# Kernel tuning notes

Measured on AMD Instinct MI355X. Metric: run time of the kernel, lower is better.

## Reference

```python
import jax, jax.numpy as jnp
import numpy as np

B, S, H = 512, 100, 768
LAMB = 0.8

def setup_inputs() -> dict:
    key = jax.random.key(0)
    k1, k2, k3, k4 = jax.random.split(key, 4)
    scale = 1.0 / np.sqrt(H)
    return {
        "sent_vec": jax.random.normal(k1, (B, S, H), dtype=jnp.float32),
        "mask_cls": jnp.ones((B, S), dtype=jnp.int32),
        "W_cont": jax.random.normal(k2, (1, H), dtype=jnp.float32) * scale,
        "W_sim": jax.random.normal(k3, (H, H), dtype=jnp.float32) * scale,
        "W_rel": jax.random.normal(k4, (H, H), dtype=jnp.float32) * scale,
        "b_matrix": jnp.zeros((1, 1), dtype=jnp.float32),
    }

def reference(sent_vec, mask_cls, W_cont, W_sim, W_rel, b_matrix):
    # sent_vec: [B,S,H], mask_cls: [B,S] (all ones -> true_dim == S)
    m = mask_cls.astype(sent_vec.dtype)                       # [B,S]
    mask2 = m[:, :, None] * m[:, None, :]                     # mask_my_own [B,S,S]

    # Score_Cont[b,i,j] = W_cont . sent_vec[b,i]
    cont = jnp.einsum('h,bih->bi', W_cont[0], sent_vec)       # [B,S]
    # Score_Sim[b,i,j] = sent_i W_sim sent_j^T, masked
    sim = jnp.einsum('bih,hk,bjk->bij', sent_vec, W_sim, sent_vec) * mask2
    # Score_rel[b,i,j] = sent_i W_rel d_rep, masked
    d_rep = sent_vec.mean(axis=1)                             # [B,H]
    rel = jnp.einsum('bih,hk,bk->bi', sent_vec, W_rel, d_rep) # [B,S]

    q = jax.nn.sigmoid(rel[:, :, None] * mask2 + cont[:, :, None] + sim + b_matrix[0, 0])
    q = q * mask2                                             # [B,S,S]

    # D = diag(column sums of q); q @ D^{-1} divides columns by sum_vec
    sum_vec = q.sum(axis=1)                                   # [B,S]
    qD = q / sum_vec[:, None, :]                              # [B,S,S]

    I = jnp.eye(S, dtype=q.dtype)
    M = I[None, :, :] - LAMB * qD                             # [B,S,S]
    y = jnp.full((B, S, 1), 1.0 / S, dtype=q.dtype)
    # Final_score = (1-lamb) * inv(I - lamb q D^-1) @ y  (solve == inverse@mm)
    score = (1.0 - LAMB) * jnp.linalg.solve(M, y)[:, :, 0]    # [B,S]
    return score
```

## Files before the change

kernel.cpp:

```cpp
#include <hip/hip_runtime.h>
#include <math.h>

#define BB 512
#define SS 100
#define HH 768

typedef __bf16 bf16x8 __attribute__((ext_vector_type(8)));
typedef __bf16 bf16x4 __attribute__((ext_vector_type(4)));
typedef float f32x4 __attribute__((ext_vector_type(4)));
typedef float f32x16 __attribute__((ext_vector_type(16)));

__device__ __forceinline__ void gld16(const void* g, void* l) {
    __builtin_amdgcn_global_load_lds((const __attribute__((address_space(1))) char*)g,
                                     (__attribute__((address_space(3))) char*)l, 16, 0, 0);
}

__global__ __launch_bounds__(256) void k_drep(const float* __restrict__ X,
                                              float* __restrict__ drep) {
    int b = blockIdx.x, g = blockIdx.y;
    int lane = threadIdx.x & 63, w = threadIdx.x >> 6;
    const float4* xb = (const float4*)(X + (size_t)b * SS * HH);
    int c4 = g * 64 + lane;
    float4 s = {0.f, 0.f, 0.f, 0.f};
    for (int r = w; r < SS; r += 4) {
        float4 v = xb[r * 192 + c4];
        s.x += v.x; s.y += v.y; s.z += v.z; s.w += v.w;
    }
    __shared__ float4 red[4][64];
    red[w][lane] = s;
    __syncthreads();
    if (w == 0) {
        float4 a0 = red[0][lane], a1 = red[1][lane], a2 = red[2][lane], a3 = red[3][lane];
        float4 o;
        o.x = (a0.x + a1.x + a2.x + a3.x) * (1.0f / SS);
        o.y = (a0.y + a1.y + a2.y + a3.y) * (1.0f / SS);
        o.z = (a0.z + a1.z + a2.z + a3.z) * (1.0f / SS);
        o.w = (a0.w + a1.w + a2.w + a3.w) * (1.0f / SS);
        ((float4*)(drep + (size_t)b * HH))[c4] = o;
    }
}

__global__ __launch_bounds__(256) void k_gemm_nt(const float* __restrict__ A,
                                                 const float* __restrict__ Bm,
                                                 float* __restrict__ C,
                                                 int N, int K) {
    __shared__ float As[64 * 20];
    __shared__ float Bs[64 * 20];
    int tid = threadIdx.x;
    int ty = tid >> 4, tx = tid & 15;
    int m0 = blockIdx.y * 64, n0 = blockIdx.x * 64;
    int lr = tid >> 2, lc = (tid & 3) * 4;
    float acc[4][4] = {};
    for (int kt = 0; kt < K; kt += 16) {
        *(float4*)(As + lr * 20 + lc) = *(const float4*)(A + (size_t)(m0 + lr) * K + kt + lc);
        *(float4*)(Bs + lr * 20 + lc) = *(const float4*)(Bm + (size_t)(n0 + lr) * K + kt + lc);
        __syncthreads();
        #pragma unroll
        for (int k = 0; k < 16; k += 2) {
            float2 ar[4], br[4];
            #pragma unroll
            for (int ii = 0; ii < 4; ++ii) ar[ii] = *(const float2*)(As + (ty + 16 * ii) * 20 + k);
            #pragma unroll
            for (int jj = 0; jj < 4; ++jj) br[jj] = *(const float2*)(Bs + (tx + 16 * jj) * 20 + k);
            #pragma unroll
            for (int ii = 0; ii < 4; ++ii)
                #pragma unroll
                for (int jj = 0; jj < 4; ++jj)
                    acc[ii][jj] = fmaf(ar[ii].y, br[jj].y, fmaf(ar[ii].x, br[jj].x, acc[ii][jj]));
        }
        __syncthreads();
    }
    #pragma unroll
    for (int ii = 0; ii < 4; ++ii)
        #pragma unroll
        for (int jj = 0; jj < 4; ++jj)
            C[(size_t)(m0 + ty + 16 * ii) * N + n0 + tx + 16 * jj] = acc[ii][jj];
}

__global__ __launch_bounds__(256) void k_splitw(const float* __restrict__ W,
                                                __bf16* __restrict__ th,
                                                __bf16* __restrict__ tl) {
    __shared__ float tile[32][33];
    int bn = blockIdx.x * 32, bk = blockIdx.y * 32;
    int tx = threadIdx.x & 31, ty = threadIdx.x >> 5;
    for (int r = ty; r < 32; r += 8)
        tile[r][tx] = W[(size_t)(bk + r) * HH + bn + tx];
    __syncthreads();
    for (int r = ty; r < 32; r += 8) {
        float v = tile[tx][r];
        __bf16 hv = (__bf16)v;
        size_t idx = (size_t)(bn + r) * HH + bk + tx;
        th[idx] = hv;
        tl[idx] = (__bf16)(v - (float)hv);
    }
}

__global__ __launch_bounds__(512) void k_split_contrel(const float* __restrict__ X,
                                                       const float* __restrict__ Wc,
                                                       const float* __restrict__ tmat,
                                                       const float* __restrict__ bmat,
                                                       __bf16* __restrict__ Xh,
                                                       __bf16* __restrict__ Xl,
                                                       float* __restrict__ avec,
                                                       int b_off) {
    __shared__ float4 u4[192];
    int lb = blockIdx.x, half = blockIdx.y;
    int b = b_off + lb;
    int tid = threadIdx.x, lane = tid & 63, w = tid >> 6;
    for (int c = tid; c < 192; c += 512) {
        float4 wc = ((const float4*)Wc)[c];
        float4 tm = ((const float4*)(tmat + (size_t)b * HH))[c];
        float4 o = {wc.x + tm.x, wc.y + tm.y, wc.z + tm.z, wc.w + tm.w};
        u4[c] = o;
    }
    __syncthreads();
    float b00 = bmat[0];
    const float4* xb = (const float4*)(X + (size_t)b * SS * HH);
    bf16x4* xh4 = (bf16x4*)(Xh + (size_t)lb * SS * HH);
    bf16x4* xl4 = (bf16x4*)(Xl + (size_t)lb * SS * HH);
    int rend = half * 50 + 50;
    for (int r = half * 50 + w; r < rend; r += 8) {
        float s = 0.f;
        #pragma unroll
        for (int cc = 0; cc < 3; ++cc) {
            int c = cc * 64 + lane;
            float4 v = xb[r * 192 + c];
            float4 uu = u4[c];
            s = fmaf(v.x, uu.x, fmaf(v.y, uu.y, fmaf(v.z, uu.z, fmaf(v.w, uu.w, s))));
            bf16x4 hv, lv;
            hv[0] = (__bf16)v.x; lv[0] = (__bf16)(v.x - (float)hv[0]);
            hv[1] = (__bf16)v.y; lv[1] = (__bf16)(v.y - (float)hv[1]);
            hv[2] = (__bf16)v.z; lv[2] = (__bf16)(v.z - (float)hv[2]);
            hv[3] = (__bf16)v.w; lv[3] = (__bf16)(v.w - (float)hv[3]);
            xh4[r * 192 + c] = hv;
            xl4[r * 192 + c] = lv;
        }
        #pragma unroll
        for (int off = 32; off > 0; off >>= 1) s += __shfl_down(s, off);
        if (lane == 0) avec[(size_t)b * SS + r] = s + b00;
    }
}

__global__ __launch_bounds__(256) void k_gemm1_mfma(const __bf16* __restrict__ Ah_g,
                                                    const __bf16* __restrict__ Al_g,
                                                    const __bf16* __restrict__ Bh_g,
                                                    const __bf16* __restrict__ Bl_g,
                                                    __bf16* __restrict__ Yh,
                                                    __bf16* __restrict__ Yl) {
    __shared__ __align__(16) __bf16 lds[4 * 4096];
    __bf16* As_h = lds;
    __bf16* As_l = lds + 4096;
    __bf16* Bs_h = lds + 8192;
    __bf16* Bs_l = lds + 12288;
    const int tid = threadIdx.x;
    const int wave = tid >> 6, lane = tid & 63;
    const int wy = wave >> 1, wx = wave & 1;
    const size_t m0 = (size_t)blockIdx.y * 128;
    const int n0 = blockIdx.x * 128;

    const int srow = wave * 32 + (lane >> 2);
    const int scol = ((lane & 3) ^ ((lane >> 3) & 3)) * 8;
    const int lds_base = wave * 1024;

    const int arow = wy * 64 + (lane & 31);
    const int brow = wx * 64 + (lane & 31);
    const int sw = (lane >> 1) & 3;

    f32x16 acc[2][2] = {};
    for (int kt = 0; kt < HH; kt += 32) {
        const size_t ga0 = (m0 + srow) * HH + kt + scol;
        const size_t ga1 = ga0 + (size_t)16 * HH;
        const size_t gb0 = (size_t)(n0 + srow) * HH + kt + scol;
        const size_t gb1 = gb0 + (size_t)16 * HH;
        gld16(Ah_g + ga0, As_h + lds_base);
        gld16(Ah_g + ga1, As_h + lds_base + 512);
        gld16(Al_g + ga0, As_l + lds_base);
        gld16(Al_g + ga1, As_l + lds_base + 512);
        gld16(Bh_g + gb0, Bs_h + lds_base);
        gld16(Bh_g + gb1, Bs_h + lds_base + 512);
        gld16(Bl_g + gb0, Bs_l + lds_base);
        gld16(Bl_g + gb1, Bs_l + lds_base + 512);
        __syncthreads();
        #pragma unroll
        for (int kh = 0; kh < 2; ++kh) {
            const int ko = (((kh << 1) + (lane >> 5)) ^ sw) << 3;
            bf16x8 fah[2], fal[2], fbh[2], fbl[2];
            #pragma unroll
            for (int t = 0; t < 2; ++t) {
                fah[t] = *(const bf16x8*)(As_h + (arow + t * 32) * 32 + ko);
                fal[t] = *(const bf16x8*)(As_l + (arow + t * 32) * 32 + ko);
                fbh[t] = *(const bf16x8*)(Bs_h + (brow + t * 32) * 32 + ko);
                fbl[t] = *(const bf16x8*)(Bs_l + (brow + t * 32) * 32 + ko);
            }
            #pragma unroll
            for (int ti = 0; ti < 2; ++ti)
                #pragma unroll
                for (int tj = 0; tj < 2; ++tj) {
                    acc[ti][tj] = __builtin_amdgcn_mfma_f32_32x32x16_bf16(fal[ti], fbh[tj], acc[ti][tj], 0, 0, 0);
                    acc[ti][tj] = __builtin_amdgcn_mfma_f32_32x32x16_bf16(fah[ti], fbl[tj], acc[ti][tj], 0, 0, 0);
                    acc[ti][tj] = __builtin_amdgcn_mfma_f32_32x32x16_bf16(fah[ti], fbh[tj], acc[ti][tj], 0, 0, 0);
                }
        }
        __syncthreads();
    }
    const int rbase = 4 * (lane >> 5);
    const int colb = lane & 31;
    #pragma unroll
    for (int ti = 0; ti < 2; ++ti) {
        #pragma unroll
        for (int tj = 0; tj < 2; ++tj) {
            int col = n0 + wx * 64 + tj * 32 + colb;
            #pragma unroll
            for (int r = 0; r < 16; ++r) {
                int row = wy * 64 + ti * 32 + (r & 3) + 8 * (r >> 2) + rbase;
                float v = acc[ti][tj][r];
                __bf16 hv = (__bf16)v;
                size_t idx = (m0 + row) * HH + col;
                Yh[idx] = hv;
                Yl[idx] = (__bf16)(v - (float)hv);
            }
        }
    }
}

__global__ __launch_bounds__(256) void k_gemm2_mfma(const __bf16* __restrict__ Yh,
                                                    const __bf16* __restrict__ Yl,
                                                    const __bf16* __restrict__ Xh,
                                                    const __bf16* __restrict__ Xl,
                                                    const float* __restrict__ avec,
                                                    float* __restrict__ q, int b_off) {
    __shared__ __align__(16) __bf16 lds[4 * 4096];
    __shared__ float av_s[SS];
    __bf16* As_h = lds;
    __bf16* As_l = lds + 4096;
    __bf16* Bs_h = lds + 8192;
    __bf16* Bs_l = lds + 12288;
    const int bl = blockIdx.x;
    const int b = b_off + bl;
    const __bf16* Ah_g = Yh + (size_t)bl * SS * HH;
    const __bf16* Al_g = Yl + (size_t)bl * SS * HH;
    const __bf16* Bh_g = Xh + (size_t)bl * SS * HH;
    const __bf16* Bl_g = Xl + (size_t)bl * SS * HH;
    const int tid = threadIdx.x;
    const int wave = tid >> 6, lane = tid & 63;
    const int wy = wave >> 1, wx = wave & 1;
    if (tid < SS) av_s[tid] = avec[(size_t)b * SS + tid];

    const int srow_raw = wave * 32 + (lane >> 2);
    const int scol = ((lane & 3) ^ ((lane >> 3) & 3)) * 8;
    const int lds_base = wave * 1024;
    const int r0 = srow_raw < SS ? srow_raw : SS - 1;
    const int r1 = (srow_raw + 16) < SS ? (srow_raw + 16) : SS - 1;

    const int arow = wy * 64 + (lane & 31);
    const int brow = wx * 64 + (lane & 31);
    const int sw = (lane >> 1) & 3;

    f32x16 acc[2][2] = {};
    for (int kt = 0; kt < HH; kt += 32) {
        const size_t ga0 = (size_t)r0 * HH + kt + scol;
        const size_t ga1 = (size_t)r1 * HH + kt + scol;
        gld16(Ah_g + ga0, As_h + lds_base);
        gld16(Ah_g + ga1, As_h + lds_base + 512);
        gld16(Al_g + ga0, As_l + lds_base);
        gld16(Al_g + ga1, As_l + lds_base + 512);
        gld16(Bh_g + ga0, Bs_h + lds_base);
        gld16(Bh_g + ga1, Bs_h + lds_base + 512);
        gld16(Bl_g + ga0, Bs_l + lds_base);
        gld16(Bl_g + ga1, Bs_l + lds_base + 512);
        __syncthreads();
        #pragma unroll
        for (int kh = 0; kh < 2; ++kh) {
            const int ko = (((kh << 1) + (lane >> 5)) ^ sw) << 3;
            bf16x8 fah[2], fal[2], fbh[2], fbl[2];
            #pragma unroll
            for (int t = 0; t < 2; ++t) {
                fah[t] = *(const bf16x8*)(As_h + (arow + t * 32) * 32 + ko);
                fal[t] = *(const bf16x8*)(As_l + (arow + t * 32) * 32 + ko);
                fbh[t] = *(const bf16x8*)(Bs_h + (brow + t * 32) * 32 + ko);
                fbl[t] = *(const bf16x8*)(Bs_l + (brow + t * 32) * 32 + ko);
            }
            #pragma unroll
            for (int ti = 0; ti < 2; ++ti)
                #pragma unroll
                for (int tj = 0; tj < 2; ++tj) {
                    acc[ti][tj] = __builtin_amdgcn_mfma_f32_32x32x16_bf16(fal[ti], fbh[tj], acc[ti][tj], 0, 0, 0);
                    acc[ti][tj] = __builtin_amdgcn_mfma_f32_32x32x16_bf16(fah[ti], fbl[tj], acc[ti][tj], 0, 0, 0);
                    acc[ti][tj] = __builtin_amdgcn_mfma_f32_32x32x16_bf16(fah[ti], fbh[tj], acc[ti][tj], 0, 0, 0);
                }
        }
        __syncthreads();
    }
    float* qb = q + (size_t)b * SS * SS;
    const int rbase = 4 * (lane >> 5);
    const int colb = lane & 31;
    #pragma unroll
    for (int ti = 0; ti < 2; ++ti) {
        #pragma unroll
        for (int tj = 0; tj < 2; ++tj) {
            int j = wx * 64 + tj * 32 + colb;
            if (j >= SS) continue;
            #pragma unroll
            for (int r = 0; r < 16; ++r) {
                int i = wy * 64 + ti * 32 + (r & 3) + 8 * (r >> 2) + rbase;
                if (i >= SS) continue;
                float v = acc[ti][tj][r] + av_s[i];
                qb[(size_t)i * SS + j] = 1.0f / (1.0f + __expf(-v));
            }
        }
    }
}

__global__ __launch_bounds__(128) void k_solve(const float* __restrict__ q,
                                               float* __restrict__ out) {
    __shared__ __align__(16) float m[SS * SS];
    __shared__ __align__(16) float csinv[SS];
    __shared__ __align__(16) float x0[SS], x1[SS];
    int b = blockIdx.x, tid = threadIdx.x;
    const float* qb = q + (size_t)b * SS * SS;
    for (int e4 = tid; e4 < SS * SS / 4; e4 += 128)
        *(float4*)(m + e4 * 4) = *(const float4*)(qb + (size_t)e4 * 4);
    __syncthreads();
    if (tid < SS) {
        float s = 0.f;
        for (int i = 0; i < SS; ++i) s += m[i * SS + tid];
        csinv[tid] = 0.8f / s;
        x0[tid] = 1.0f / SS;
    }
    __syncthreads();
    float4 mreg[25];
    if (tid < SS) {
        #pragma unroll
        for (int j4 = 0; j4 < 25; ++j4) {
            float4 mv = *(const float4*)(m + tid * SS + j4 * 4);
            float4 cv = *(const float4*)(csinv + j4 * 4);
            mreg[j4].x = mv.x * cv.x;
            mreg[j4].y = mv.y * cv.y;
            mreg[j4].z = mv.z * cv.z;
            mreg[j4].w = mv.w * cv.w;
        }
    } else {
        #pragma unroll
        for (int j4 = 0; j4 < 25; ++j4) mreg[j4] = float4{0, 0, 0, 0};
    }
    __syncthreads();
    #pragma unroll 1
    for (int it = 0; it < 56; ++it) {
        const float* xr = (it & 1) ? x1 : x0;
        float* xw = (it & 1) ? x0 : x1;
        if (tid < SS) {
            float sx = 0.f, sy = 0.f, sz = 0.f, sw = 0.f;
            #pragma unroll
            for (int j4 = 0; j4 < 25; ++j4) {
                float4 xv = *(const float4*)(xr + j4 * 4);
                sx = fmaf(mreg[j4].x, xv.x, sx);
                sy = fmaf(mreg[j4].y, xv.y, sy);
                sz = fmaf(mreg[j4].z, xv.z, sz);
                sw = fmaf(mreg[j4].w, xv.w, sw);
            }
            xw[tid] = 0.002f + ((sx + sy) + (sz + sw));
        }
        __syncthreads();
    }
    if (tid < SS) out[(size_t)b * SS + tid] = x0[tid];
}

extern "C" void kernel_launch(void* const* d_in, const int* in_sizes, int n_in,
                              void* d_out, int out_size, void* d_ws, size_t ws_size,
                              hipStream_t stream) {
    (void)in_sizes; (void)n_in; (void)out_size;
    const float* X    = (const float*)d_in[0];
    const float* Wc   = (const float*)d_in[2];
    const float* Wsim = (const float*)d_in[3];
    const float* Wrel = (const float*)d_in[4];
    const float* bmat = (const float*)d_in[5];
    float* out = (float*)d_out;

    char* ws = (char*)d_ws;
    size_t off = 0;
    float*  qbuf = (float*)(ws + off);  off += (size_t)BB * SS * SS * 4;
    float*  drep = (float*)(ws + off);  off += (size_t)BB * HH * 4;
    float*  tmat = (float*)(ws + off);  off += (size_t)BB * HH * 4;
    float*  avec = (float*)(ws + off);  off += (size_t)BB * SS * 4;
    __bf16* Wth  = (__bf16*)(ws + off); off += (size_t)HH * HH * 2;
    __bf16* Wtl  = (__bf16*)(ws + off); off += (size_t)HH * HH * 2;

    int CB = 512;
    while (CB > 128 && off + 4 * (size_t)CB * SS * HH * 2 > ws_size) CB >>= 1;
    size_t xsz = (size_t)CB * SS * HH * 2;
    __bf16* Xh = (__bf16*)(ws + off); off += xsz;
    __bf16* Xl = (__bf16*)(ws + off); off += xsz;
    __bf16* Yh = (__bf16*)(ws + off); off += xsz;
    __bf16* Yl = (__bf16*)(ws + off); off += xsz;

    k_drep<<<dim3(BB, 3), 256, 0, stream>>>(X, drep);
    k_gemm_nt<<<dim3(HH / 64, BB / 64), 256, 0, stream>>>(drep, Wrel, tmat, HH, HH);
    k_splitw<<<dim3(HH / 32, HH / 32), 256, 0, stream>>>(Wsim, Wth, Wtl);

    for (int c = 0; c < BB; c += CB) {
        k_split_contrel<<<dim3(CB, 2), 512, 0, stream>>>(X + (size_t)c * SS * HH, Wc, tmat, bmat, Xh, Xl, avec, c);
        k_gemm1_mfma<<<dim3(HH / 128, CB * SS / 128), 256, 0, stream>>>(Xh, Xl, Wth, Wtl, Yh, Yl);
        k_gemm2_mfma<<<CB, 256, 0, stream>>>(Yh, Yl, Xh, Xl, avec, qbuf, c);
    }
    k_solve<<<BB, 128, 0, stream>>>(qbuf, out);
}
```

Baseline: 722.8 us.

## Double-buffer LDS tiles in both MFMA GEMM kernels to overlap loads with compute

Both split-bf16 GEMM kernels now allocate two LDS stage buffers and issue the async global-to-LDS loads for the next K tile before running the MFMA work on the current tile. This removes one barrier per K step and is meant to hide global load latency behind matrix math. LDS use per block doubles to 64KB, which may lower occupancy. Correctness depends on the barrier at the end of each iteration also covering completion of the outstanding async LDS loads.

```diff
diff --git a/kernel.cpp b/kernel.cpp
--- a/kernel.cpp
+++ b/kernel.cpp
@@ -147,11 +147,7 @@
                                                     const __bf16* __restrict__ Bl_g,
                                                     __bf16* __restrict__ Yh,
                                                     __bf16* __restrict__ Yl) {
-    __shared__ __align__(16) __bf16 lds[4 * 4096];
-    __bf16* As_h = lds;
-    __bf16* As_l = lds + 4096;
-    __bf16* Bs_h = lds + 8192;
-    __bf16* Bs_l = lds + 12288;
+    __shared__ __align__(16) __bf16 lds[2 * 4 * 4096];
     const int tid = threadIdx.x;
     const int wave = tid >> 6, lane = tid & 63;
     const int wy = wave >> 1, wx = wave & 1;
@@ -167,20 +163,27 @@
     const int sw = (lane >> 1) & 3;
 
     f32x16 acc[2][2] = {};
-    for (int kt = 0; kt < HH; kt += 32) {
+
+    auto stage = [&](int buf, int kt) {
+        __bf16* base = lds + buf * 16384;
         const size_t ga0 = (m0 + srow) * HH + kt + scol;
         const size_t ga1 = ga0 + (size_t)16 * HH;
         const size_t gb0 = (size_t)(n0 + srow) * HH + kt + scol;
         const size_t gb1 = gb0 + (size_t)16 * HH;
-        gld16(Ah_g + ga0, As_h + lds_base);
-        gld16(Ah_g + ga1, As_h + lds_base + 512);
-        gld16(Al_g + ga0, As_l + lds_base);
-        gld16(Al_g + ga1, As_l + lds_base + 512);
-        gld16(Bh_g + gb0, Bs_h + lds_base);
-        gld16(Bh_g + gb1, Bs_h + lds_base + 512);
-        gld16(Bl_g + gb0, Bs_l + lds_base);
-        gld16(Bl_g + gb1, Bs_l + lds_base + 512);
-        __syncthreads();
+        gld16(Ah_g + ga0, base + lds_base);
+        gld16(Ah_g + ga1, base + lds_base + 512);
+        gld16(Al_g + ga0, base + 4096 + lds_base);
+        gld16(Al_g + ga1, base + 4096 + lds_base + 512);
+        gld16(Bh_g + gb0, base + 8192 + lds_base);
+        gld16(Bh_g + gb1, base + 8192 + lds_base + 512);
+        gld16(Bl_g + gb0, base + 12288 + lds_base);
+        gld16(Bl_g + gb1, base + 12288 + lds_base + 512);
+    };
+    auto compute = [&](int buf) {
+        const __bf16* As_h = lds + buf * 16384;
+        const __bf16* As_l = As_h + 4096;
+        const __bf16* Bs_h = As_h + 8192;
+        const __bf16* Bs_l = As_h + 12288;
         #pragma unroll
         for (int kh = 0; kh < 2; ++kh) {
             const int ko = (((kh << 1) + (lane >> 5)) ^ sw) << 3;
@@ -201,8 +204,19 @@
                     acc[ti][tj] = __builtin_amdgcn_mfma_f32_32x32x16_bf16(fah[ti], fbh[tj], acc[ti][tj], 0, 0, 0);
                 }
         }
+    };
+
+    stage(0, 0);
+    __syncthreads();
+    int cur = 0;
+    for (int kt = 32; kt < HH; kt += 32) {
+        stage(cur ^ 1, kt);
+        compute(cur);
         __syncthreads();
-    }
+        cur ^= 1;
+    }
+    compute(cur);
+
     const int rbase = 4 * (lane >> 5);
     const int colb = lane & 31;
     #pragma unroll
@@ -229,12 +243,8 @@
                                                     const __bf16* __restrict__ Xl,
                                                     const float* __restrict__ avec,
                                                     float* __restrict__ q, int b_off) {
-    __shared__ __align__(16) __bf16 lds[4 * 4096];
+    __shared__ __align__(16) __bf16 lds[2 * 4 * 4096];
     __shared__ float av_s[SS];
-    __bf16* As_h = lds;
-    __bf16* As_l = lds + 4096;
-    __bf16* Bs_h = lds + 8192;
-    __bf16* Bs_l = lds + 12288;
     const int bl = blockIdx.x;
     const int b = b_off + bl;
     const __bf16* Ah_g = Yh + (size_t)bl * SS * HH;
@@ -257,18 +267,25 @@
     const int sw = (lane >> 1) & 3;
 
     f32x16 acc[2][2] = {};
-    for (int kt = 0; kt < HH; kt += 32) {
+
+    auto stage = [&](int buf, int kt) {
+        __bf16* base = lds + buf * 16384;
         const size_t ga0 = (size_t)r0 * HH + kt + scol;
         const size_t ga1 = (size_t)r1 * HH + kt + scol;
-        gld16(Ah_g + ga0, As_h + lds_base);
-        gld16(Ah_g + ga1, As_h + lds_base + 512);
-        gld16(Al_g + ga0, As_l + lds_base);
-        gld16(Al_g + ga1, As_l + lds_base + 512);
-        gld16(Bh_g + ga0, Bs_h + lds_base);
-        gld16(Bh_g + ga1, Bs_h + lds_base + 512);
-        gld16(Bl_g + ga0, Bs_l + lds_base);
-        gld16(Bl_g + ga1, Bs_l + lds_base + 512);
-        __syncthreads();
+        gld16(Ah_g + ga0, base + lds_base);
+        gld16(Ah_g + ga1, base + lds_base + 512);
+        gld16(Al_g + ga0, base + 4096 + lds_base);
+        gld16(Al_g + ga1, base + 4096 + lds_base + 512);
+        gld16(Bh_g + ga0, base + 8192 + lds_base);
+        gld16(Bh_g + ga1, base + 8192 + lds_base + 512);
+        gld16(Bl_g + ga0, base + 12288 + lds_base);
+        gld16(Bl_g + ga1, base + 12288 + lds_base + 512);
+    };
+    auto compute = [&](int buf) {
+        const __bf16* As_h = lds + buf * 16384;
+        const __bf16* As_l = As_h + 4096;
+        const __bf16* Bs_h = As_h + 8192;
+        const __bf16* Bs_l = As_h + 12288;
         #pragma unroll
         for (int kh = 0; kh < 2; ++kh) {
             const int ko = (((kh << 1) + (lane >> 5)) ^ sw) << 3;
@@ -289,8 +306,19 @@
                     acc[ti][tj] = __builtin_amdgcn_mfma_f32_32x32x16_bf16(fah[ti], fbh[tj], acc[ti][tj], 0, 0, 0);
                 }
         }
+    };
+
+    stage(0, 0);
+    __syncthreads();
+    int cur = 0;
+    for (int kt = 32; kt < HH; kt += 32) {
+        stage(cur ^ 1, kt);
+        compute(cur);
         __syncthreads();
-    }
+        cur ^= 1;
+    }
+    compute(cur);
+
     float* qb = q + (size_t)b * SS * SS;
     const int rbase = 4 * (lane >> 5);
     const int colb = lane & 31;
```

Result: no change. 722.5 us (-0.0%).
